# Performance work log

Measured on AMD Instinct MI355X. Metric: run time of the kernel, lower is better.

The kernel has to match this reference:

```python
import jax, jax.numpy as jnp
import numpy as np

B, E, C, M, H = 4, 8, 512, 1024, 4096

def setup_inputs() -> dict:
    key = jax.random.key(0)
    k1, k2, k3, k4, k5 = jax.random.split(key, 5)
    s = 1.0 / np.sqrt(M)
    return {
        "x": jax.random.normal(k1, (B, E, C, M), dtype=jnp.float32),
        "fc1_weight": jax.random.normal(k2, (E, H, M), dtype=jnp.float32) * s,
        "fc1_bias": jax.random.normal(k3, (E, 1, H), dtype=jnp.float32) * 0.02,
        "fc2_weight": jax.random.normal(k4, (E, H, M), dtype=jnp.float32) * (1.0 / np.sqrt(H)),
        "fc2_bias": jax.random.normal(k5, (E, 1, M), dtype=jnp.float32) * 0.02,
    }

def reference(x, fc1_weight, fc1_bias, fc2_weight, fc2_bias):
    # x: [B, E, C, M] -> [E, B*C, M]
    b, e, c, m = x.shape
    xe = jnp.transpose(x, (1, 0, 2, 3)).reshape(e, b * c, m)
    # fc1: [E,T,M] @ [E,M,H] (fp32 grouped GEMM with bias)
    h = jnp.einsum('etm,ehm->eth', xe.astype(jnp.float32), fc1_weight.astype(jnp.float32)) + fc1_bias.astype(jnp.float32)
    h = jax.nn.relu(h)
    # fc2: [E,T,H] @ [E,H,M] + bias (dropout is identity)
    o = jnp.einsum('eth,ehm->etm', h, fc2_weight) + fc2_bias
    o = o.reshape(e, b, c, m)
    return jnp.transpose(o, (1, 0, 2, 3))
```

## Files before the change

### kernel.cpp

```cpp
#include <hip/hip_runtime.h>
#include <hip/hip_bf16.h>

typedef __bf16 bf16x8 __attribute__((ext_vector_type(8)));
typedef __bf16 bf16x4 __attribute__((ext_vector_type(4)));
typedef float  f32x4  __attribute__((ext_vector_type(4)));

constexpr int Ee = 8, Cc = 512, Mm = 1024, Hh = 4096, Tt = 2048;

__device__ __forceinline__ void async16(void* lds, const void* g) {
  __builtin_amdgcn_global_load_lds(
      (const __attribute__((address_space(1))) void*)g,
      (__attribute__((address_space(3))) void*)lds, 16, 0, 0);
}

#define FENCE() asm volatile("" ::: "memory")
#define BARRIER() do { FENCE(); __builtin_amdgcn_s_barrier(); FENCE(); } while (0)

__device__ __forceinline__ int xcd_swz(int id, int n) {
  const int q = n >> 3, r = n & 7;
  const int x = id & 7, k = id >> 3;
  return (x < r ? x * (q + 1) : r * (q + 1) + (x - r) * q) + k;
}

__device__ __forceinline__ void gemm256(
    const __bf16* __restrict__ aT, const __bf16* __restrict__ bT, const int K,
    __bf16 (*Ab)[2][128][64], __bf16 (*Bb)[2][128][64],
    f32x4 (&acc)[8][4]) {
  const int tid = threadIdx.x;
  const int lane = tid & 63, wid = tid >> 6;
  const int wr = wid >> 2, wcn = wid & 3;
  const int l8 = lane >> 3;
  const int colSwzE = (((lane & 7) ^ l8) << 3);
  const int NT = K >> 6;

  int pblk[2];
  pblk[0] = (lane >> 4) ^ (lane & 7);
  pblk[1] = (4 + (lane >> 4)) ^ (lane & 7);

  bf16x8 aF[8][2];
  bf16x8 bF[2][2];

  auto STAGE = [&](int s, int u) {
    if (s >= NT) return;
    const int d = s & 1;
    if (u < 2) {
      const __bf16* src = aT + (size_t)(u * 128 + wid * 16 + l8) * K + s * 64 + colSwzE;
#pragma unroll
      for (int i = 0; i < 2; ++i)
        async16(&Ab[d][u][wid * 16 + i * 8][0], src + (size_t)(i * 8) * K);
    } else {
      const __bf16* src = bT + (size_t)((u - 2) * 128 + wid * 16 + l8) * K + s * 64 + colSwzE;
#pragma unroll
      for (int i = 0; i < 2; ++i)
        async16(&Bb[d][u - 2][wid * 16 + i * 8][0], src + (size_t)(i * 8) * K);
    }
  };

  STAGE(0, 0); STAGE(0, 1); STAGE(0, 2); STAGE(0, 3);
  STAGE(1, 0); STAGE(1, 1);
  asm volatile("s_waitcnt vmcnt(4)" ::: "memory");
  BARRIER();

  for (int t = 0; t < NT; ++t) {
    const int d = t & 1;
    const char* pa = (const char*)&Ab[d][wr][0][0];
    const char* pb = (const char*)&Bb[d][wcn >> 1][0][0];
    const int brow = (wcn & 1) * 64;

    STAGE(t + 1, 2); STAGE(t + 1, 3);

#pragma unroll
    for (int mi = 0; mi < 8; ++mi)
#pragma unroll
      for (int kh = 0; kh < 2; ++kh)
        aF[mi][kh] = *(const bf16x8*)(pa + (mi * 16 + (lane & 15)) * 128 + pblk[kh] * 16);
#pragma unroll
    for (int ni = 0; ni < 2; ++ni)
#pragma unroll
      for (int kh = 0; kh < 2; ++kh)
        bF[ni][kh] = *(const bf16x8*)(pb + (brow + ni * 16 + (lane & 15)) * 128 + pblk[kh] * 16);

    BARRIER();

    STAGE(t + 2, 0); STAGE(t + 2, 1);

    __builtin_amdgcn_s_setprio(1);
#pragma unroll
    for (int mi = 0; mi < 8; ++mi)
#pragma unroll
      for (int ni = 0; ni < 2; ++ni)
#pragma unroll
        for (int kh = 0; kh < 2; ++kh)
          acc[mi][ni] = __builtin_amdgcn_mfma_f32_16x16x32_bf16(bF[ni][kh], aF[mi][kh], acc[mi][ni], 0, 0, 0);
    __builtin_amdgcn_s_setprio(0);

#pragma unroll
    for (int ni = 0; ni < 2; ++ni)
#pragma unroll
      for (int kh = 0; kh < 2; ++kh)
        bF[ni][kh] = *(const bf16x8*)(pb + (brow + (2 + ni) * 16 + (lane & 15)) * 128 + pblk[kh] * 16);

    __builtin_amdgcn_s_setprio(1);
#pragma unroll
    for (int mi = 0; mi < 8; ++mi)
#pragma unroll
      for (int ni = 0; ni < 2; ++ni)
#pragma unroll
        for (int kh = 0; kh < 2; ++kh)
          acc[mi][2 + ni] = __builtin_amdgcn_mfma_f32_16x16x32_bf16(bF[ni][kh], aF[mi][kh], acc[mi][2 + ni], 0, 0, 0);
    __builtin_amdgcn_s_setprio(0);

    if (t < NT - 2) { asm volatile("s_waitcnt vmcnt(4)" ::: "memory"); }
    else            { asm volatile("s_waitcnt vmcnt(0)" ::: "memory"); }
    BARRIER();
  }
}

__global__ __launch_bounds__(512, 2) void fc1g_kernel(
    const __bf16* __restrict__ xb, int eOffA,
    const __bf16* __restrict__ w1b, int eOffB,
    const float* __restrict__ b1, __bf16* __restrict__ hb,
    int e0, int t_base, int tcap, int nbT) {
  __shared__ __bf16 Ab[2][2][128][64];
  __shared__ __bf16 Bb[2][2][128][64];
  const int nbN = Hh / 256;
  const int id = xcd_swz(blockIdx.x, gridDim.x);
  const int z = id / (nbN * nbT);
  const int rm = id % (nbN * nbT);
  const int tblk = (rm / nbN) * 256, nblk = (rm % nbN) * 256;
  const int lane = threadIdx.x & 63, wid = threadIdx.x >> 6;
  const int wr = wid >> 2, wcn = wid & 3;

  const __bf16* aT = xb + ((size_t)(eOffA + z) * Tt + t_base + tblk) * Mm;
  const __bf16* bT = w1b + ((size_t)(eOffB + z) * Hh + nblk) * Mm;

  f32x4 acc[8][4];
#pragma unroll
  for (int i = 0; i < 8; ++i)
#pragma unroll
    for (int j = 0; j < 4; ++j) acc[i][j] = (f32x4){0.f, 0.f, 0.f, 0.f};

  gemm256(aT, bT, Mm, Ab, Bb, acc);

  const float* bias = b1 + (size_t)(e0 + z) * Hh;
#pragma unroll
  for (int ni = 0; ni < 4; ++ni) {
    const int n0 = nblk + wcn * 64 + ni * 16 + ((lane >> 4) << 2);
    const f32x4 b4 = *(const f32x4*)(bias + n0);
#pragma unroll
    for (int mi = 0; mi < 8; ++mi) {
      const int trow = tblk + wr * 128 + mi * 16 + (lane & 15);
      f32x4 v = acc[mi][ni];
      bf16x4 o;
#pragma unroll
      for (int rr = 0; rr < 4; ++rr) {
        float f = v[rr] + b4[rr];
        o[rr] = (__bf16)(f > 0.f ? f : 0.f);
      }
      *(bf16x4*)(hb + ((size_t)z * tcap + trow) * Hh + n0) = o;
    }
  }
}

__global__ __launch_bounds__(512, 2) void fc2g_kernel(
    const __bf16* __restrict__ hb, int tcap,
    const __bf16* __restrict__ w2t, int eOffB,
    const float* __restrict__ b2, float* __restrict__ out,
    int e0, int t_base, int nbT) {
  __shared__ __bf16 Ab[2][2][128][64];
  __shared__ __bf16 Bb[2][2][128][64];
  const int nbN = Mm / 256;
  const int id = xcd_swz(blockIdx.x, gridDim.x);
  const int z = id / (nbN * nbT);
  const int rm = id % (nbN * nbT);
  const int tblk = (rm / nbN) * 256, nblk = (rm % nbN) * 256;
  const int lane = threadIdx.x & 63, wid = threadIdx.x >> 6;
  const int wr = wid >> 2, wcn = wid & 3;
  const int e = e0 + z;

  const __bf16* aT = hb + ((size_t)z * tcap + tblk) * Hh;
  const __bf16* bT = w2t + ((size_t)(eOffB + z) * Mm + nblk) * Hh;

  f32x4 acc[8][4];
#pragma unroll
  for (int i = 0; i < 8; ++i)
#pragma unroll
    for (int j = 0; j < 4; ++j) acc[i][j] = (f32x4){0.f, 0.f, 0.f, 0.f};

  gemm256(aT, bT, Hh, Ab, Bb, acc);

  const float* bias = b2 + (size_t)e * Mm;
#pragma unroll
  for (int ni = 0; ni < 4; ++ni) {
    const int m0 = nblk + wcn * 64 + ni * 16 + ((lane >> 4) << 2);
    const f32x4 b4 = *(const f32x4*)(bias + m0);
#pragma unroll
    for (int mi = 0; mi < 8; ++mi) {
      const int t = t_base + tblk + wr * 128 + mi * 16 + (lane & 15);
      const int bb = t >> 9, cc = t & 511;
      f32x4 v = acc[mi][ni];
#pragma unroll
      for (int rr = 0; rr < 4; ++rr) v[rr] += b4[rr];
      *(f32x4*)(out + ((((size_t)bb * Ee + e) * Cc + cc) << 10) + m0) = v;
    }
  }
}

__global__ __launch_bounds__(256) void cvt_x_kernel(
    const float* __restrict__ x, __bf16* __restrict__ xb, int e0) {
  size_t idx8 = (size_t)blockIdx.x * 256 + threadIdx.x;
  int m8 = (int)(idx8 & 127);
  int t = (int)((idx8 >> 7) & 2047);
  int z = (int)(idx8 >> 18);
  int b = t >> 9, c = t & 511, e = e0 + z;
  const float* src = x + ((((size_t)b * Ee + e) * Cc + c) << 10) + (m8 << 3);
  f32x4 v0 = *(const f32x4*)src;
  f32x4 v1 = *(const f32x4*)(src + 4);
  bf16x8 o;
  o[0] = (__bf16)v0[0]; o[1] = (__bf16)v0[1]; o[2] = (__bf16)v0[2]; o[3] = (__bf16)v0[3];
  o[4] = (__bf16)v1[0]; o[5] = (__bf16)v1[1]; o[6] = (__bf16)v1[2]; o[7] = (__bf16)v1[3];
  *(bf16x8*)(xb + (idx8 << 3)) = o;
}

__global__ __launch_bounds__(256) void cvt_lin_kernel(
    const float* __restrict__ in, __bf16* __restrict__ outb) {
  size_t i8 = (size_t)blockIdx.x * 256 + threadIdx.x;
  const float* src = in + (i8 << 3);
  f32x4 v0 = *(const f32x4*)src;
  f32x4 v1 = *(const f32x4*)(src + 4);
  bf16x8 o;
  o[0] = (__bf16)v0[0]; o[1] = (__bf16)v0[1]; o[2] = (__bf16)v0[2]; o[3] = (__bf16)v0[3];
  o[4] = (__bf16)v1[0]; o[5] = (__bf16)v1[1]; o[6] = (__bf16)v1[2]; o[7] = (__bf16)v1[3];
  *(bf16x8*)(outb + (i8 << 3)) = o;
}

__global__ __launch_bounds__(256) void tr_w2_kernel(
    const float* __restrict__ w2, __bf16* __restrict__ w2t, int e0) {
  __shared__ __bf16 tile[64][68];
  const int z = blockIdx.z, e = e0 + z;
  const int m0 = blockIdx.x * 64, h0 = blockIdx.y * 64;
  const int tid = threadIdx.x;
  const int cg = tid & 15, rg = tid >> 4;
#pragma unroll
  for (int p = 0; p < 4; ++p) {
    int hl = rg + p * 16;
    f32x4 v = *(const f32x4*)(w2 + (((size_t)e * Hh + h0 + hl) << 10) + m0 + (cg << 2));
#pragma unroll
    for (int i = 0; i < 4; ++i) tile[(cg << 2) + i][hl] = (__bf16)v[i];
  }
  __syncthreads();
#pragma unroll
  for (int p = 0; p < 4; ++p) {
    int ml = rg + p * 16;
    uint2 pk = *(const uint2*)(&tile[ml][cg << 2]);
    *(uint2*)(w2t + ((size_t)z * Mm + m0 + ml) * Hh + h0 + (cg << 2)) = pk;
  }
}

extern "C" void kernel_launch(void* const* d_in, const int* in_sizes, int n_in,
                              void* d_out, int out_size, void* d_ws, size_t ws_size,
                              hipStream_t stream) {
  const float* x  = (const float*)d_in[0];
  const float* w1 = (const float*)d_in[1];
  const float* b1 = (const float*)d_in[2];
  const float* w2 = (const float*)d_in[3];
  const float* b2 = (const float*)d_in[4];
  float* out = (float*)d_out;

  const size_t xbS = (size_t)Tt * Mm * 2;
  const size_t w1S = (size_t)Hh * Mm * 2;
  const size_t w2S = (size_t)Mm * Hh * 2;
  const size_t hbS = (size_t)Tt * Hh * 2;
  char* ws = (char*)d_ws;

  if (ws_size >= Ee * (xbS + w1S + w2S + hbS)) {
    __bf16* xb  = (__bf16*)ws;
    __bf16* w1b = (__bf16*)(ws + Ee * xbS);
    __bf16* w2t = (__bf16*)(ws + Ee * (xbS + w1S));
    __bf16* hb  = (__bf16*)(ws + Ee * (xbS + w1S + w2S));
    cvt_x_kernel<<<Ee * 1024, 256, 0, stream>>>(x, xb, 0);
    cvt_lin_kernel<<<Ee * 2048, 256, 0, stream>>>(w1, w1b);
    tr_w2_kernel<<<dim3(Mm / 64, Hh / 64, Ee), 256, 0, stream>>>(w2, w2t, 0);
    fc1g_kernel<<<(Hh / 256) * (Tt / 256) * Ee, 512, 0, stream>>>(xb, 0, w1b, 0, b1, hb, 0, 0, Tt, Tt / 256);
    fc2g_kernel<<<(Mm / 256) * (Tt / 256) * Ee, 512, 0, stream>>>(hb, Tt, w2t, 0, b2, out, 0, 0, Tt / 256);
  } else if (ws_size >= Ee * (xbS + w1S + w2S) + hbS) {
    __bf16* xb  = (__bf16*)ws;
    __bf16* w1b = (__bf16*)(ws + Ee * xbS);
    __bf16* w2t = (__bf16*)(ws + Ee * (xbS + w1S));
    __bf16* hb  = (__bf16*)(ws + Ee * (xbS + w1S + w2S));
    int Gh = (int)((ws_size - Ee * (xbS + w1S + w2S)) / hbS);
    if (Gh > Ee) Gh = Ee;
    cvt_x_kernel<<<Ee * 1024, 256, 0, stream>>>(x, xb, 0);
    cvt_lin_kernel<<<Ee * 2048, 256, 0, stream>>>(w1, w1b);
    tr_w2_kernel<<<dim3(Mm / 64, Hh / 64, Ee), 256, 0, stream>>>(w2, w2t, 0);
    for (int e0 = 0; e0 < Ee; e0 += Gh) {
      int g = (Ee - e0) < Gh ? (Ee - e0) : Gh;
      fc1g_kernel<<<(Hh / 256) * (Tt / 256) * g, 512, 0, stream>>>(xb, e0, w1b, e0, b1, hb, e0, 0, Tt, Tt / 256);
      fc2g_kernel<<<(Mm / 256) * (Tt / 256) * g, 512, 0, stream>>>(hb, Tt, w2t, e0, b2, out, e0, 0, Tt / 256);
    }
  } else if (ws_size >= xbS + w1S + w2S + hbS) {
    int G = (int)(ws_size / (xbS + w1S + w2S + hbS));
    if (G > Ee) G = Ee;
    __bf16* xb  = (__bf16*)ws;
    __bf16* w1b = (__bf16*)(ws + (size_t)G * xbS);
    __bf16* w2t = (__bf16*)(ws + (size_t)G * (xbS + w1S));
    __bf16* hb  = (__bf16*)(ws + (size_t)G * (xbS + w1S + w2S));
    for (int e0 = 0; e0 < Ee; e0 += G) {
      int g = (Ee - e0) < G ? (Ee - e0) : G;
      cvt_x_kernel<<<g * 1024, 256, 0, stream>>>(x, xb, e0);
      cvt_lin_kernel<<<g * 2048, 256, 0, stream>>>(w1 + (size_t)e0 * Hh * Mm, w1b);
      tr_w2_kernel<<<dim3(Mm / 64, Hh / 64, g), 256, 0, stream>>>(w2, w2t, e0);
      fc1g_kernel<<<(Hh / 256) * (Tt / 256) * g, 512, 0, stream>>>(xb, 0, w1b, 0, b1, hb, e0, 0, Tt, Tt / 256);
      fc2g_kernel<<<(Mm / 256) * (Tt / 256) * g, 512, 0, stream>>>(hb, Tt, w2t, 0, b2, out, e0, 0, Tt / 256);
    }
  } else {
    __bf16* xb  = (__bf16*)ws;
    __bf16* w1b = (__bf16*)(ws + xbS);
    __bf16* w2t = (__bf16*)(ws + xbS + w1S);
    __bf16* hb  = (__bf16*)(ws + xbS + w1S + w2S);
    size_t rem = ws_size > (xbS + w1S + w2S) ? ws_size - (xbS + w1S + w2S) : 0;
    int Tc = (int)(rem / ((size_t)Hh * 2)) & ~255;
    if (Tc > Tt) Tc = Tt;
    if (Tc < 256) Tc = 256;
    for (int e0 = 0; e0 < Ee; ++e0) {
      cvt_x_kernel<<<1024, 256, 0, stream>>>(x, xb, e0);
      cvt_lin_kernel<<<2048, 256, 0, stream>>>(w1 + (size_t)e0 * Hh * Mm, w1b);
      tr_w2_kernel<<<dim3(Mm / 64, Hh / 64, 1), 256, 0, stream>>>(w2, w2t, e0);
      for (int t0 = 0; t0 < Tt; t0 += Tc) {
        int tc = (Tt - t0) < Tc ? (Tt - t0) : Tc;
        fc1g_kernel<<<(Hh / 256) * (tc / 256), 512, 0, stream>>>(xb, 0, w1b, 0, b1, hb, e0, t0, Tc, tc / 256);
        fc2g_kernel<<<(Mm / 256) * (tc / 256), 512, 0, stream>>>(hb, Tc, w2t, 0, b2, out, e0, t0, tc / 256);
      }
    }
  }
}
```

Before: 426.8 us.

## Split GEMM main loop into four interleaved phases of LDS reads, async loads and MFMA

Restructures the K-loop of the shared 256x256 bf16 GEMM into four quadrant phases. Each phase issues one async global-to-LDS stage, reads only the A/B fragments it needs, and runs a quarter of the MFMAs, with barriers between phases. The B fragments are kept in two separate register sets. The aim is to interleave memory traffic with matrix math more finely, in the style of a ping-pong schedule, so load latency hides behind compute. In exchange it adds several barriers per iteration and more B-fragment registers.

```diff
diff --git a/kernel.cpp b/kernel.cpp
--- a/kernel.cpp
+++ b/kernel.cpp
@@ -38,7 +38,8 @@
   pblk[1] = (4 + (lane >> 4)) ^ (lane & 7);
 
   bf16x8 aF[8][2];
-  bf16x8 bF[2][2];
+  bf16x8 bFa[2][2];
+  bf16x8 bFb[2][2];
 
   auto STAGE = [&](int s, int u) {
     if (s >= NT) return;
@@ -67,10 +68,8 @@
     const char* pb = (const char*)&Bb[d][wcn >> 1][0][0];
     const int brow = (wcn & 1) * 64;
 
-    STAGE(t + 1, 2); STAGE(t + 1, 3);
-
-#pragma unroll
-    for (int mi = 0; mi < 8; ++mi)
+#pragma unroll
+    for (int mi = 0; mi < 4; ++mi)
 #pragma unroll
       for (int kh = 0; kh < 2; ++kh)
         aF[mi][kh] = *(const bf16x8*)(pa + (mi * 16 + (lane & 15)) * 128 + pblk[kh] * 16);
@@ -78,38 +77,70 @@
     for (int ni = 0; ni < 2; ++ni)
 #pragma unroll
       for (int kh = 0; kh < 2; ++kh)
-        bF[ni][kh] = *(const bf16x8*)(pb + (brow + ni * 16 + (lane & 15)) * 128 + pblk[kh] * 16);
-
-    BARRIER();
-
-    STAGE(t + 2, 0); STAGE(t + 2, 1);
-
+        bFa[ni][kh] = *(const bf16x8*)(pb + (brow + ni * 16 + (lane & 15)) * 128 + pblk[kh] * 16);
+    STAGE(t + 1, 2);
+    asm volatile("s_waitcnt lgkmcnt(8)" ::: "memory");
+    BARRIER();
+    asm volatile("s_waitcnt lgkmcnt(0)" ::: "memory");
     __builtin_amdgcn_s_setprio(1);
 #pragma unroll
-    for (int mi = 0; mi < 8; ++mi)
+    for (int mi = 0; mi < 4; ++mi)
 #pragma unroll
       for (int ni = 0; ni < 2; ++ni)
 #pragma unroll
         for (int kh = 0; kh < 2; ++kh)
-          acc[mi][ni] = __builtin_amdgcn_mfma_f32_16x16x32_bf16(bF[ni][kh], aF[mi][kh], acc[mi][ni], 0, 0, 0);
+          acc[mi][ni] = __builtin_amdgcn_mfma_f32_16x16x32_bf16(bFa[ni][kh], aF[mi][kh], acc[mi][ni], 0, 0, 0);
     __builtin_amdgcn_s_setprio(0);
+    BARRIER();
+
+#pragma unroll
+    for (int mi = 0; mi < 4; ++mi)
+#pragma unroll
+      for (int kh = 0; kh < 2; ++kh)
+        aF[4 + mi][kh] = *(const bf16x8*)(pa + ((4 + mi) * 16 + (lane & 15)) * 128 + pblk[kh] * 16);
+    STAGE(t + 1, 3);
+    BARRIER();
+    asm volatile("s_waitcnt lgkmcnt(0)" ::: "memory");
+    __builtin_amdgcn_s_setprio(1);
+#pragma unroll
+    for (int mi = 0; mi < 4; ++mi)
+#pragma unroll
+      for (int ni = 0; ni < 2; ++ni)
+#pragma unroll
+        for (int kh = 0; kh < 2; ++kh)
+          acc[4 + mi][ni] = __builtin_amdgcn_mfma_f32_16x16x32_bf16(bFa[ni][kh], aF[4 + mi][kh], acc[4 + mi][ni], 0, 0, 0);
+    __builtin_amdgcn_s_setprio(0);
+    BARRIER();
 
 #pragma unroll
     for (int ni = 0; ni < 2; ++ni)
 #pragma unroll
       for (int kh = 0; kh < 2; ++kh)
-        bF[ni][kh] = *(const bf16x8*)(pb + (brow + (2 + ni) * 16 + (lane & 15)) * 128 + pblk[kh] * 16);
-
+        bFb[ni][kh] = *(const bf16x8*)(pb + (brow + (2 + ni) * 16 + (lane & 15)) * 128 + pblk[kh] * 16);
+    STAGE(t + 2, 0);
+    BARRIER();
+    asm volatile("s_waitcnt lgkmcnt(0)" ::: "memory");
     __builtin_amdgcn_s_setprio(1);
 #pragma unroll
-    for (int mi = 0; mi < 8; ++mi)
+    for (int mi = 0; mi < 4; ++mi)
 #pragma unroll
       for (int ni = 0; ni < 2; ++ni)
 #pragma unroll
         for (int kh = 0; kh < 2; ++kh)
-          acc[mi][2 + ni] = __builtin_amdgcn_mfma_f32_16x16x32_bf16(bF[ni][kh], aF[mi][kh], acc[mi][2 + ni], 0, 0, 0);
+          acc[4 + mi][2 + ni] = __builtin_amdgcn_mfma_f32_16x16x32_bf16(bFb[ni][kh], aF[4 + mi][kh], acc[4 + mi][2 + ni], 0, 0, 0);
     __builtin_amdgcn_s_setprio(0);
-
+    BARRIER();
+
+    STAGE(t + 2, 1);
+    __builtin_amdgcn_s_setprio(1);
+#pragma unroll
+    for (int mi = 0; mi < 4; ++mi)
+#pragma unroll
+      for (int ni = 0; ni < 2; ++ni)
+#pragma unroll
+        for (int kh = 0; kh < 2; ++kh)
+          acc[mi][2 + ni] = __builtin_amdgcn_mfma_f32_16x16x32_bf16(bFb[ni][kh], aF[mi][kh], acc[mi][2 + ni], 0, 0, 0);
+    __builtin_amdgcn_s_setprio(0);
     if (t < NT - 2) { asm volatile("s_waitcnt vmcnt(4)" ::: "memory"); }
     else            { asm volatile("s_waitcnt vmcnt(0)" ::: "memory"); }
     BARRIER();
```

Result: slower. 445.4 us (+4.4%).

## Fuse prep conversions into one kernel and reorder GEMM tile rasterization

Applied to the files above, without the earlier changes.

Merges the three preprocessing kernels (x conversion, w1 conversion, w2 transpose) into a single launch that dispatches on block index, removing two launches and the tail gaps between them. Also changes the tile index mapping in both GEMMs so that consecutive blocks walk along the token dimension for a fixed output column block. Adjacent blocks therefore share the same weight tile instead of the same activation tile, which is meant to change L2 reuse patterns. The branchy fused kernel mixes block types with different LDS needs, so every block reserves the transpose's shared tile.

```diff
diff --git a/kernel.cpp b/kernel.cpp
--- a/kernel.cpp
+++ b/kernel.cpp
@@ -127,7 +127,7 @@
   const int id = xcd_swz(blockIdx.x, gridDim.x);
   const int z = id / (nbN * nbT);
   const int rm = id % (nbN * nbT);
-  const int tblk = (rm / nbN) * 256, nblk = (rm % nbN) * 256;
+  const int tblk = (rm % nbT) * 256, nblk = (rm / nbT) * 256;
   const int lane = threadIdx.x & 63, wid = threadIdx.x >> 6;
   const int wr = wid >> 2, wcn = wid & 3;
 
@@ -173,7 +173,7 @@
   const int id = xcd_swz(blockIdx.x, gridDim.x);
   const int z = id / (nbN * nbT);
   const int rm = id % (nbN * nbT);
-  const int tblk = (rm / nbN) * 256, nblk = (rm % nbN) * 256;
+  const int tblk = (rm % nbT) * 256, nblk = (rm / nbT) * 256;
   const int lane = threadIdx.x & 63, wid = threadIdx.x >> 6;
   const int wr = wid >> 2, wcn = wid & 3;
   const int e = e0 + z;
@@ -202,6 +202,59 @@
 #pragma unroll
       for (int rr = 0; rr < 4; ++rr) v[rr] += b4[rr];
       *(f32x4*)(out + ((((size_t)bb * Ee + e) * Cc + cc) << 10) + m0) = v;
+    }
+  }
+}
+
+__global__ __launch_bounds__(256) void prep_all_kernel(
+    const float* __restrict__ x, const float* __restrict__ w1,
+    const float* __restrict__ w2, __bf16* __restrict__ xb,
+    __bf16* __restrict__ w1b, __bf16* __restrict__ w2t) {
+  __shared__ __bf16 tile[64][68];
+  const int bid = blockIdx.x;
+  if (bid < 8192) {
+    size_t idx8 = (size_t)bid * 256 + threadIdx.x;
+    int m8 = (int)(idx8 & 127);
+    int t = (int)((idx8 >> 7) & 2047);
+    int z = (int)(idx8 >> 18);
+    int b = t >> 9, c = t & 511;
+    const float* src = x + ((((size_t)b * Ee + z) * Cc + c) << 10) + (m8 << 3);
+    f32x4 v0 = *(const f32x4*)src;
+    f32x4 v1 = *(const f32x4*)(src + 4);
+    bf16x8 o;
+    o[0] = (__bf16)v0[0]; o[1] = (__bf16)v0[1]; o[2] = (__bf16)v0[2]; o[3] = (__bf16)v0[3];
+    o[4] = (__bf16)v1[0]; o[5] = (__bf16)v1[1]; o[6] = (__bf16)v1[2]; o[7] = (__bf16)v1[3];
+    *(bf16x8*)(xb + (idx8 << 3)) = o;
+  } else if (bid < 24576) {
+    size_t i8 = (size_t)(bid - 8192) * 256 + threadIdx.x;
+    const float* src = w1 + (i8 << 3);
+    f32x4 v0 = *(const f32x4*)src;
+    f32x4 v1 = *(const f32x4*)(src + 4);
+    bf16x8 o;
+    o[0] = (__bf16)v0[0]; o[1] = (__bf16)v0[1]; o[2] = (__bf16)v0[2]; o[3] = (__bf16)v0[3];
+    o[4] = (__bf16)v1[0]; o[5] = (__bf16)v1[1]; o[6] = (__bf16)v1[2]; o[7] = (__bf16)v1[3];
+    *(bf16x8*)(w1b + (i8 << 3)) = o;
+  } else {
+    const int tb = bid - 24576;
+    const int z = tb >> 10;
+    const int rem = tb & 1023;
+    const int m0 = (rem & 15) * 64;
+    const int h0 = (rem >> 4) * 64;
+    const int tid = threadIdx.x;
+    const int cg = tid & 15, rg = tid >> 4;
+#pragma unroll
+    for (int p = 0; p < 4; ++p) {
+      int hl = rg + p * 16;
+      f32x4 v = *(const f32x4*)(w2 + (((size_t)z * Hh + h0 + hl) << 10) + m0 + (cg << 2));
+#pragma unroll
+      for (int i = 0; i < 4; ++i) tile[(cg << 2) + i][hl] = (__bf16)v[i];
+    }
+    __syncthreads();
+#pragma unroll
+    for (int p = 0; p < 4; ++p) {
+      int ml = rg + p * 16;
+      uint2 pk = *(const uint2*)(&tile[ml][cg << 2]);
+      *(uint2*)(w2t + ((size_t)z * Mm + m0 + ml) * Hh + h0 + (cg << 2)) = pk;
     }
   }
 }
@@ -278,9 +331,7 @@
     __bf16* w1b = (__bf16*)(ws + Ee * xbS);
     __bf16* w2t = (__bf16*)(ws + Ee * (xbS + w1S));
     __bf16* hb  = (__bf16*)(ws + Ee * (xbS + w1S + w2S));
-    cvt_x_kernel<<<Ee * 1024, 256, 0, stream>>>(x, xb, 0);
-    cvt_lin_kernel<<<Ee * 2048, 256, 0, stream>>>(w1, w1b);
-    tr_w2_kernel<<<dim3(Mm / 64, Hh / 64, Ee), 256, 0, stream>>>(w2, w2t, 0);
+    prep_all_kernel<<<32768, 256, 0, stream>>>(x, w1, w2, xb, w1b, w2t);
     fc1g_kernel<<<(Hh / 256) * (Tt / 256) * Ee, 512, 0, stream>>>(xb, 0, w1b, 0, b1, hb, 0, 0, Tt, Tt / 256);
     fc2g_kernel<<<(Mm / 256) * (Tt / 256) * Ee, 512, 0, stream>>>(hb, Tt, w2t, 0, b2, out, 0, 0, Tt / 256);
   } else if (ws_size >= Ee * (xbS + w1S + w2S) + hbS) {
@@ -290,9 +341,7 @@
     __bf16* hb  = (__bf16*)(ws + Ee * (xbS + w1S + w2S));
     int Gh = (int)((ws_size - Ee * (xbS + w1S + w2S)) / hbS);
     if (Gh > Ee) Gh = Ee;
-    cvt_x_kernel<<<Ee * 1024, 256, 0, stream>>>(x, xb, 0);
-    cvt_lin_kernel<<<Ee * 2048, 256, 0, stream>>>(w1, w1b);
-    tr_w2_kernel<<<dim3(Mm / 64, Hh / 64, Ee), 256, 0, stream>>>(w2, w2t, 0);
+    prep_all_kernel<<<32768, 256, 0, stream>>>(x, w1, w2, xb, w1b, w2t);
     for (int e0 = 0; e0 < Ee; e0 += Gh) {
       int g = (Ee - e0) < Gh ? (Ee - e0) : Gh;
       fc1g_kernel<<<(Hh / 256) * (Tt / 256) * g, 512, 0, stream>>>(xb, e0, w1b, e0, b1, hb, e0, 0, Tt, Tt / 256);
```

Result: slower. 488.0 us (+14.3%).
